# Optimization experiments

Measured on AMD Instinct MI355X. Metric: run time of the kernel, lower is better.

## Reference

```python
import jax, jax.numpy as jnp
import numpy as np

MAX_NUM_BINS = 200
BIN_SIZE = 500
NUM_NEIGHBORS = 5
DIST_MULT = 0.1


def setup_inputs() -> dict:
    key = jax.random.key(0)
    k1, k2 = jax.random.split(key)
    points = jax.random.normal(k1, (2, 5000, 128), dtype=jnp.float32)
    rotations = jax.random.normal(k2, (128, MAX_NUM_BINS // 2), dtype=jnp.float32)
    return {"points": points, "rotations": rotations}


def reference(points, rotations):
    # points: [B, N, D], rotations: [D, max_num_bins//2]
    B, N, D = points.shape
    nbins = N // BIN_SIZE  # module requires N % BIN_SIZE == 0

    # LSH bin assignment: project onto nbins//2 random directions, sign-split into nbins bins
    mul = jnp.einsum('bnd,dh->bnh', points, rotations[:, :nbins // 2])  # [B,N,nbins//2]
    cmul = jnp.concatenate([mul, -mul], axis=-1)                        # [B,N,nbins]
    bin_idx = jnp.argmax(cmul, axis=-1)                                 # [B,N]
    # equal-size bins via argsort of bin id (matches tf argsort+reshape)
    bins_split = jnp.argsort(bin_idx, axis=-1).reshape(B, nbins, BIN_SIZE)  # [B,nbins,S]

    # gather points per bin
    parts = jnp.take_along_axis(points, bins_split.reshape(B, N, 1), axis=1)
    parts = parts.reshape(B, nbins, BIN_SIZE, D)

    # per-bin pairwise distance -> gaussian kernel
    na = jnp.sum(parts * parts, axis=-1)                                # [B,nbins,S]
    gram = jnp.einsum('bcid,bcjd->bcij', parts, parts)                  # [B,nbins,S,S]
    dist = jnp.sqrt(jnp.maximum(na[..., :, None] - 2.0 * gram + na[..., None, :], 1e-6))
    dm = jnp.exp(-DIST_MULT * dist)                                     # [B,nbins,S,S]

    # top-k neighbors within each bin
    vals, idx = jax.lax.top_k(dm, NUM_NEIGHBORS)                        # [B,nbins,S,K]

    # map local bin indices back to global point indices
    bs_flat = bins_split.reshape(B * nbins, BIN_SIZE)
    dst = jnp.take_along_axis(bs_flat, idx.reshape(B * nbins, BIN_SIZE * NUM_NEIGHBORS), axis=1)
    dst = dst.reshape(B, nbins, BIN_SIZE, NUM_NEIGHBORS)
    src = jnp.broadcast_to(bins_split[..., None], dst.shape)
    bidx = jnp.broadcast_to(jnp.arange(B)[:, None, None, None], dst.shape)

    # scatter-add into dense [B,N,N] (sparse.add sums duplicate entries)
    out = jnp.zeros((B, N, N), dtype=points.dtype)
    out = out.at[bidx.reshape(-1), src.reshape(-1), dst.reshape(-1)].add(vals.reshape(-1))
    return out
```

## Files before the change

kernel.cpp:

```cpp
#include <hip/hip_runtime.h>
#include <cfloat>
#include <math.h>

#define NPTS   5000
#define BATCH  2
#define DIM    128
#define NBINS  10
#define BINSZ  500
#define TOPK   5
#define ROTCOLS 100

#define KB_PTS 64
#define KB_STR 129
__global__ void k_bins(const float* __restrict__ pts, const float* __restrict__ rot,
                       int* __restrict__ bin_idx, double* __restrict__ na) {
    __shared__ float P[KB_PTS * KB_STR];
    __shared__ float rotL[DIM * 5];
    int tid = threadIdx.x;
    for (int f = tid; f < DIM * 5; f += 256)
        rotL[f] = rot[(f / 5) * ROTCOLS + (f % 5)];

    int p0  = blockIdx.x * KB_PTS;
    int npb = min(KB_PTS, BATCH * NPTS - p0);

    for (int f = tid; f < npb * DIM; f += 256) {
        int r = f >> 7, d = f & 127;
        P[r * KB_STR + d] = pts[(size_t)(p0 + r) * DIM + d];
    }
    __syncthreads();

    int p = tid >> 2;
    int s = tid & 3;
    double acc[5] = {0., 0., 0., 0., 0.};
    double sq = 0.;
    const float* row = &P[p * KB_STR + s * 32];
    for (int j = 0; j < 32; ++j) {
        double v = (double)row[j];
        sq += v * v;
        int d = s * 32 + j;
#pragma unroll
        for (int h = 0; h < 5; ++h) acc[h] += v * (double)rotL[d * 5 + h];
    }
#pragma unroll
    for (int m = 1; m < 4; m <<= 1) {
#pragma unroll
        for (int h = 0; h < 5; ++h) acc[h] += __shfl_xor(acc[h], m, 4);
        sq += __shfl_xor(sq, m, 4);
    }
    if (s == 0 && p < npb) {
        double best = acc[0]; int bc = 0;
#pragma unroll
        for (int c = 1; c < NBINS; ++c) {
            double v = (c < 5) ? acc[c] : -acc[c - 5];
            if (v > best) { best = v; bc = c; }
        }
        bin_idx[p0 + p] = bc;
        na[p0 + p] = sq;
    }
}

__global__ void k_sort(const int* __restrict__ bin_idx, int* __restrict__ order) {
    const int b = blockIdx.x;
    const int t = threadIdx.x;
    const int NPT = (NPTS + 255) / 256;
    int start = t * NPT;
    int end   = min(NPTS, start + NPT);

    int cnt[NBINS];
#pragma unroll
    for (int c = 0; c < NBINS; ++c) cnt[c] = 0;
    for (int i = start; i < end; ++i) {
        int c = bin_idx[b * NPTS + i];
#pragma unroll
        for (int k = 0; k < NBINS; ++k) cnt[k] += (c == k);
    }

    __shared__ int hist[NBINS * 256];
#pragma unroll
    for (int c = 0; c < NBINS; ++c) hist[c * 256 + t] = cnt[c];
    __syncthreads();

    int base = t * NBINS;
    int s = 0;
#pragma unroll
    for (int k = 0; k < NBINS; ++k) s += hist[base + k];
    __shared__ int scan[256];
    scan[t] = s;
    __syncthreads();
    for (int off = 1; off < 256; off <<= 1) {
        int v = (t >= off) ? scan[t - off] : 0;
        __syncthreads();
        scan[t] += v;
        __syncthreads();
    }
    int run = scan[t] - s;
#pragma unroll
    for (int k = 0; k < NBINS; ++k) { int h = hist[base + k]; hist[base + k] = run; run += h; }
    __syncthreads();

    int ofs[NBINS];
#pragma unroll
    for (int c = 0; c < NBINS; ++c) ofs[c] = hist[c * 256 + t];
    for (int i = start; i < end; ++i) {
        int c = bin_idx[b * NPTS + i];
        int pos = 0;
#pragma unroll
        for (int k = 0; k < NBINS; ++k) {
            if (c == k) pos = ofs[k];
            ofs[k] += (c == k);
        }
        order[b * NPTS + pos] = i;
    }
}

#define RT    16
#define NRT   32
#define CTILE 64
#define RSTRD 130
#define CSTR  132
#define NCT   8
#define ROWQ  (NPTS/4)

__launch_bounds__(256, 3)
__global__ void k_chunks(const float* __restrict__ pts, const double* __restrict__ na,
                         const int* __restrict__ order, float* __restrict__ out) {
    __shared__ double rowPd[RT * RSTRD];
    __shared__ float  colP[CTILE * CSTR];
    __shared__ double naC[CTILE];
    __shared__ double naRs[RT];
    __shared__ int    ordR[RT];

    int blk   = blockIdx.x;
    int rt    = blk & (NRT - 1);
    int chunk = blk >> 5;
    int b     = chunk / NBINS;
    int c     = chunk % NBINS;
    int tid   = threadIdx.x;
    int row0  = rt * RT;
    int rowCount = min(RT, BINSZ - row0);

    const int*   ordBase = order + b * NPTS + c * BINSZ;
    const float* ptsB    = pts + (size_t)b * NPTS * DIM;

    for (int f = tid; f < rowCount * (DIM / 4); f += 256) {
        int r = f >> 5;
        int q = f & 31;
        int g = ordBase[row0 + r];
        float4 v = *(const float4*)(ptsB + (size_t)g * DIM + q * 4);
        double2 d01; d01.x = (double)v.x; d01.y = (double)v.y;
        double2 d23; d23.x = (double)v.z; d23.y = (double)v.w;
        *(double2*)(&rowPd[r * RSTRD + q * 4 + 0]) = d01;
        *(double2*)(&rowPd[r * RSTRD + q * 4 + 2]) = d23;
    }
    if (tid < rowCount) {
        int g = ordBase[row0 + tid];
        ordR[tid] = g;
        naRs[tid] = na[b * NPTS + g];
    }
    __syncthreads();

    int rg = tid >> 5;
    int cg = tid & 31;

    double naRr0 = (rg     < rowCount) ? naRs[rg]     : 0.;
    double naRr1 = (rg + 8 < rowCount) ? naRs[rg + 8] : 0.;

    double tv[2][TOPK];
    int    tl[2][TOPK];
#pragma unroll
    for (int ii = 0; ii < 2; ++ii)
#pragma unroll
        for (int k = 0; k < TOPK; ++k) { tv[ii][k] = DBL_MAX; tl[ii][k] = 0x7fffffff; }

    const int totalZ = rowCount * ROWQ;

    for (int ct = 0; ct < NCT; ++ct) {
        int col0 = ct * CTILE;
        int colCount = min(CTILE, BINSZ - col0);
        __syncthreads();
        for (int f = tid; f < colCount * (DIM / 4); f += 256) {
            int j = f >> 5;
            int q = f & 31;
            int g = ordBase[col0 + j];
            float4 v = *(const float4*)(ptsB + (size_t)g * DIM + q * 4);
            *(float4*)(&colP[j * CSTR + q * 4]) = v;
        }
        if (tid < colCount) {
            int g = ordBase[col0 + tid];
            naC[tid] = na[b * NPTS + g];
        }
        __syncthreads();

        {
            float4 z = make_float4(0.f, 0.f, 0.f, 0.f);
            int z0 = (ct * totalZ) / NCT, z1 = ((ct + 1) * totalZ) / NCT;
            for (int f = z0 + tid; f < z1; f += 256) {
                int r = f / ROWQ;
                int q = f - r * ROWQ;
                float* outRow = out + ((size_t)b * NPTS + ordR[r]) * NPTS;
                *(float4*)(outRow + 4 * q) = z;
            }
        }

        double acc00 = 0., acc01 = 0., acc10 = 0., acc11 = 0.;

        for (int q = 0; q < DIM / 4; ++q) {
            double2 a0lo = *(const double2*)(&rowPd[rg * RSTRD + q * 4 + 0]);
            double2 a0hi = *(const double2*)(&rowPd[rg * RSTRD + q * 4 + 2]);
            double2 a1lo = *(const double2*)(&rowPd[(rg + 8) * RSTRD + q * 4 + 0]);
            double2 a1hi = *(const double2*)(&rowPd[(rg + 8) * RSTRD + q * 4 + 2]);
            float4 b0 = *(const float4*)(&colP[cg * CSTR + q * 4]);
            float4 b1 = *(const float4*)(&colP[(cg + 32) * CSTR + q * 4]);
            double b00 = (double)b0.x, b01 = (double)b0.y,
                   b02 = (double)b0.z, b03 = (double)b0.w;
            double b10 = (double)b1.x, b11 = (double)b1.y,
                   b12 = (double)b1.z, b13 = (double)b1.w;
            acc00 += a0lo.x * b00 + a0lo.y * b01 + a0hi.x * b02 + a0hi.y * b03;
            acc01 += a0lo.x * b10 + a0lo.y * b11 + a0hi.x * b12 + a0hi.y * b13;
            acc10 += a1lo.x * b00 + a1lo.y * b01 + a1hi.x * b02 + a1hi.y * b03;
            acc11 += a1lo.x * b10 + a1lo.y * b11 + a1hi.x * b12 + a1hi.y * b13;
        }

#pragma unroll
        for (int jj = 0; jj < 2; ++jj) {
            int j = cg + 32 * jj;
            if (j < colCount) {
                int    cl = col0 + j;
                double nc = naC[j];
                double a0 = (jj == 0) ? acc00 : acc01;
                double a1 = (jj == 0) ? acc10 : acc11;
                double cv0 = fmax(naRr0 + nc - 2. * a0, 1e-6);
                double cv1 = fmax(naRr1 + nc - 2. * a1, 1e-6);
                int cl0 = cl, cl1 = cl;
#pragma unroll
                for (int k = 0; k < TOPK; ++k) {
                    bool lt0 = (cv0 < tv[0][k]);
                    double ov0 = tv[0][k]; int ol0 = tl[0][k];
                    if (lt0) { tv[0][k] = cv0; tl[0][k] = cl0; cv0 = ov0; cl0 = ol0; }
                    bool lt1 = (cv1 < tv[1][k]);
                    double ov1 = tv[1][k]; int ol1 = tl[1][k];
                    if (lt1) { tv[1][k] = cv1; tl[1][k] = cl1; cv1 = ov1; cl1 = ol1; }
                }
            }
        }
    }

#pragma unroll
    for (int m = 1; m < 32; m <<= 1) {
#pragma unroll
        for (int ii = 0; ii < 2; ++ii) {
            double rv[TOPK]; int rl[TOPK];
#pragma unroll
            for (int k = 0; k < TOPK; ++k) {
                rv[k] = __shfl_xor(tv[ii][k], m, 32);
                rl[k] = __shfl_xor(tl[ii][k], m, 32);
            }
#pragma unroll
            for (int k = 0; k < TOPK; ++k) {
                double cv = rv[k]; int cl = rl[k];
#pragma unroll
                for (int s = 0; s < TOPK; ++s) {
                    bool better = (cv < tv[ii][s]) || (cv == tv[ii][s] && cl < tl[ii][s]);
                    double ov = tv[ii][s]; int ol = tl[ii][s];
                    if (better) { tv[ii][s] = cv; tl[ii][s] = cl; cv = ov; cl = ol; }
                }
            }
        }
    }

    __syncthreads();

    if (cg == 0) {
#pragma unroll
        for (int ii = 0; ii < 2; ++ii) {
            int r = rg + 8 * ii;
            if (r < rowCount) {
                int src = ordR[r];
                float* outRow = out + ((size_t)b * NPTS + src) * NPTS;
#pragma unroll
                for (int k = 0; k < TOPK; ++k) {
                    double dist = sqrt(tv[ii][k]);
                    double dm   = exp(-0.1 * dist);
                    int dst = ordBase[tl[ii][k]];
                    outRow[dst] = (float)dm;
                }
            }
        }
    }
}

extern "C" void kernel_launch(void* const* d_in, const int* in_sizes, int n_in,
                              void* d_out, int out_size, void* d_ws, size_t ws_size,
                              hipStream_t stream) {
    const float* pts = (const float*)d_in[0];
    const float* rot = (const float*)d_in[1];
    float* out = (float*)d_out;

    double* na      = (double*)d_ws;
    int*    bin_idx = (int*)((char*)d_ws + 80000);
    int*    order   = (int*)((char*)d_ws + 120000);

    k_bins<<<(BATCH * NPTS + KB_PTS - 1) / KB_PTS, 256, 0, stream>>>(pts, rot, bin_idx, na);
    k_sort<<<BATCH, 256, 0, stream>>>(bin_idx, order);
    k_chunks<<<BATCH * NBINS * NRT, 256, 0, stream>>>(pts, na, order, out);
}
```

Before: 295.5 us.

## Compute per-bin Gram tiles with FP64 MFMA and merge top-k across waves

Replaces the scalar FP64 dot-product loop in the chunk kernel with v_mfma_f64_16x16x4f64 matrix instructions. Each wave computes a 16x16 tile of rows by columns. A runtime probe detects the MFMA operand layout, and a scalar fallback is kept in case the probe fails. The per-row top-k is now reduced over 16-lane shuffles and then merged across the four waves through shared memory. The aim is to cut FP64 ALU cost in the Gram computation, at the price of extra probe work, an additional barrier and a cross-wave merge step.

New measurement: 340.8 us. +15.3%, slower.

```diff
diff --git a/kernel.cpp b/kernel.cpp
--- a/kernel.cpp
+++ b/kernel.cpp
@@ -121,6 +121,8 @@
 #define NCT   8
 #define ROWQ  (NPTS/4)
 
+typedef double v4d __attribute__((ext_vector_type(4)));
+
 __launch_bounds__(256, 3)
 __global__ void k_chunks(const float* __restrict__ pts, const double* __restrict__ na,
                          const int* __restrict__ order, float* __restrict__ out) {
@@ -141,6 +143,31 @@
 
     const int*   ordBase = order + b * NPTS + c * BINSZ;
     const float* ptsB    = pts + (size_t)b * NPTS * DIM;
+
+    int lane = tid & 63;
+    int w    = tid >> 6;
+    int mm   = lane & 15;
+    int gg   = lane >> 4;
+
+    v4d pz = {0., 0., 0., 0.};
+    v4d pB = __builtin_amdgcn_mfma_f64_16x16x4f64(1.0, (double)lane, pz, 0, 0, 0);
+    v4d pA = __builtin_amdgcn_mfma_f64_16x16x4f64((double)lane, 1.0, pz, 0, 0, 0);
+    bool okB1 = true, okB2 = true, okA1 = true, okA2 = true;
+#pragma unroll
+    for (int r = 0; r < 4; ++r) {
+        okB1 = okB1 && (pB[r] == (double)(4 * mm + 96));
+        okB2 = okB2 && (pB[r] == (double)(16 * mm + 6));
+        int rowr = 4 * gg + r;
+        okA1 = okA1 && (pA[r] == (double)(4 * rowr + 96));
+        okA2 = okA2 && (pA[r] == (double)(16 * rowr + 6));
+    }
+    int aconv = __all(okA1) ? 1 : (__all(okA2) ? 2 : 0);
+    int bconv = __all(okB1) ? 1 : (__all(okB2) ? 2 : 0);
+    bool useMfma = (aconv != 0) && (bconv != 0);
+    int iA = (aconv == 2) ? (lane >> 2) : mm;
+    int kA = (aconv == 2) ? (lane & 3)  : gg;
+    int jB = (bconv == 2) ? (lane >> 2) : mm;
+    int kB = (bconv == 2) ? (lane & 3)  : gg;
 
     for (int f = tid; f < rowCount * (DIM / 4); f += 256) {
         int r = f >> 5;
@@ -159,20 +186,24 @@
     }
     __syncthreads();
 
-    int rg = tid >> 5;
-    int cg = tid & 31;
-
-    double naRr0 = (rg     < rowCount) ? naRs[rg]     : 0.;
-    double naRr1 = (rg + 8 < rowCount) ? naRs[rg + 8] : 0.;
-
-    double tv[2][TOPK];
-    int    tl[2][TOPK];
-#pragma unroll
-    for (int ii = 0; ii < 2; ++ii)
-#pragma unroll
-        for (int k = 0; k < TOPK; ++k) { tv[ii][k] = DBL_MAX; tl[ii][k] = 0x7fffffff; }
+    double naR[4];
+#pragma unroll
+    for (int i = 0; i < 4; ++i) {
+        int r = 4 * gg + i;
+        naR[i] = (r < rowCount) ? naRs[r] : 0.;
+    }
+
+    double tv[4][TOPK];
+    int    tl[4][TOPK];
+#pragma unroll
+    for (int i = 0; i < 4; ++i)
+#pragma unroll
+        for (int k = 0; k < TOPK; ++k) { tv[i][k] = DBL_MAX; tl[i][k] = 0x7fffffff; }
 
     const int totalZ = rowCount * ROWQ;
+
+    const double* aBase = &rowPd[iA * RSTRD + kA];
+    const float*  bBase = &colP[(16 * w + jB) * CSTR + kB];
 
     for (int ct = 0; ct < NCT; ++ct) {
         int col0 = ct * CTILE;
@@ -202,89 +233,120 @@
             }
         }
 
-        double acc00 = 0., acc01 = 0., acc10 = 0., acc11 = 0.;
-
-        for (int q = 0; q < DIM / 4; ++q) {
-            double2 a0lo = *(const double2*)(&rowPd[rg * RSTRD + q * 4 + 0]);
-            double2 a0hi = *(const double2*)(&rowPd[rg * RSTRD + q * 4 + 2]);
-            double2 a1lo = *(const double2*)(&rowPd[(rg + 8) * RSTRD + q * 4 + 0]);
-            double2 a1hi = *(const double2*)(&rowPd[(rg + 8) * RSTRD + q * 4 + 2]);
-            float4 b0 = *(const float4*)(&colP[cg * CSTR + q * 4]);
-            float4 b1 = *(const float4*)(&colP[(cg + 32) * CSTR + q * 4]);
-            double b00 = (double)b0.x, b01 = (double)b0.y,
-                   b02 = (double)b0.z, b03 = (double)b0.w;
-            double b10 = (double)b1.x, b11 = (double)b1.y,
-                   b12 = (double)b1.z, b13 = (double)b1.w;
-            acc00 += a0lo.x * b00 + a0lo.y * b01 + a0hi.x * b02 + a0hi.y * b03;
-            acc01 += a0lo.x * b10 + a0lo.y * b11 + a0hi.x * b12 + a0hi.y * b13;
-            acc10 += a1lo.x * b00 + a1lo.y * b01 + a1hi.x * b02 + a1hi.y * b03;
-            acc11 += a1lo.x * b10 + a1lo.y * b11 + a1hi.x * b12 + a1hi.y * b13;
-        }
-
-#pragma unroll
-        for (int jj = 0; jj < 2; ++jj) {
-            int j = cg + 32 * jj;
+        v4d accv = {0., 0., 0., 0.};
+        if (useMfma) {
+#pragma unroll
+            for (int s = 0; s < 32; ++s) {
+                double av = aBase[4 * s];
+                double bv = (double)bBase[4 * s];
+                accv = __builtin_amdgcn_mfma_f64_16x16x4f64(av, bv, accv, 0, 0, 0);
+            }
+        } else {
+            const float*  bcol = &colP[(16 * w + mm) * CSTR];
+            const double* r0 = &rowPd[(4 * gg + 0) * RSTRD];
+            const double* r1 = &rowPd[(4 * gg + 1) * RSTRD];
+            const double* r2 = &rowPd[(4 * gg + 2) * RSTRD];
+            const double* r3 = &rowPd[(4 * gg + 3) * RSTRD];
+            double s0 = 0., s1 = 0., s2 = 0., s3 = 0.;
+#pragma unroll 4
+            for (int q = 0; q < DIM; q += 4) {
+                float4 bf = *(const float4*)(&bcol[q]);
+                double b0 = (double)bf.x, b1 = (double)bf.y,
+                       b2 = (double)bf.z, b3 = (double)bf.w;
+                s0 += r0[q] * b0 + r0[q + 1] * b1 + r0[q + 2] * b2 + r0[q + 3] * b3;
+                s1 += r1[q] * b0 + r1[q + 1] * b1 + r1[q + 2] * b2 + r1[q + 3] * b3;
+                s2 += r2[q] * b0 + r2[q + 1] * b1 + r2[q + 2] * b2 + r2[q + 3] * b3;
+                s3 += r3[q] * b0 + r3[q + 1] * b1 + r3[q + 2] * b2 + r3[q + 3] * b3;
+            }
+            accv[0] = s0; accv[1] = s1; accv[2] = s2; accv[3] = s3;
+        }
+
+        {
+            int j = 16 * w + mm;
             if (j < colCount) {
                 int    cl = col0 + j;
                 double nc = naC[j];
-                double a0 = (jj == 0) ? acc00 : acc01;
-                double a1 = (jj == 0) ? acc10 : acc11;
-                double cv0 = fmax(naRr0 + nc - 2. * a0, 1e-6);
-                double cv1 = fmax(naRr1 + nc - 2. * a1, 1e-6);
-                int cl0 = cl, cl1 = cl;
-#pragma unroll
-                for (int k = 0; k < TOPK; ++k) {
-                    bool lt0 = (cv0 < tv[0][k]);
-                    double ov0 = tv[0][k]; int ol0 = tl[0][k];
-                    if (lt0) { tv[0][k] = cv0; tl[0][k] = cl0; cv0 = ov0; cl0 = ol0; }
-                    bool lt1 = (cv1 < tv[1][k]);
-                    double ov1 = tv[1][k]; int ol1 = tl[1][k];
-                    if (lt1) { tv[1][k] = cv1; tl[1][k] = cl1; cv1 = ov1; cl1 = ol1; }
+#pragma unroll
+                for (int i = 0; i < 4; ++i) {
+                    double cv = fmax(naR[i] + nc - 2. * accv[i], 1e-6);
+                    int ci = cl;
+#pragma unroll
+                    for (int k = 0; k < TOPK; ++k) {
+                        bool lt = (cv < tv[i][k]);
+                        double ov = tv[i][k]; int ol = tl[i][k];
+                        if (lt) { tv[i][k] = cv; tl[i][k] = ci; cv = ov; ci = ol; }
+                    }
                 }
             }
         }
     }
 
 #pragma unroll
-    for (int m = 1; m < 32; m <<= 1) {
-#pragma unroll
-        for (int ii = 0; ii < 2; ++ii) {
+    for (int m = 1; m < 16; m <<= 1) {
+#pragma unroll
+        for (int i = 0; i < 4; ++i) {
             double rv[TOPK]; int rl[TOPK];
 #pragma unroll
             for (int k = 0; k < TOPK; ++k) {
-                rv[k] = __shfl_xor(tv[ii][k], m, 32);
-                rl[k] = __shfl_xor(tl[ii][k], m, 32);
+                rv[k] = __shfl_xor(tv[i][k], m, 16);
+                rl[k] = __shfl_xor(tl[i][k], m, 16);
             }
 #pragma unroll
             for (int k = 0; k < TOPK; ++k) {
                 double cv = rv[k]; int cl = rl[k];
 #pragma unroll
                 for (int s = 0; s < TOPK; ++s) {
-                    bool better = (cv < tv[ii][s]) || (cv == tv[ii][s] && cl < tl[ii][s]);
-                    double ov = tv[ii][s]; int ol = tl[ii][s];
-                    if (better) { tv[ii][s] = cv; tl[ii][s] = cl; cv = ov; cl = ol; }
+                    bool better = (cv < tv[i][s]) || (cv == tv[i][s] && cl < tl[i][s]);
+                    double ov = tv[i][s]; int ol = tl[i][s];
+                    if (better) { tv[i][s] = cv; tl[i][s] = cl; cv = ov; cl = ol; }
                 }
             }
         }
     }
 
     __syncthreads();
-
-    if (cg == 0) {
-#pragma unroll
-        for (int ii = 0; ii < 2; ++ii) {
-            int r = rg + 8 * ii;
-            if (r < rowCount) {
-                int src = ordR[r];
-                float* outRow = out + ((size_t)b * NPTS + src) * NPTS;
-#pragma unroll
-                for (int k = 0; k < TOPK; ++k) {
-                    double dist = sqrt(tv[ii][k]);
-                    double dm   = exp(-0.1 * dist);
-                    int dst = ordBase[tl[ii][k]];
-                    outRow[dst] = (float)dm;
+    double* mV = rowPd;
+    int*    mI = reinterpret_cast<int*>(rowPd + 320);
+    if (mm == 0) {
+#pragma unroll
+        for (int i = 0; i < 4; ++i) {
+            int r = 4 * gg + i;
+#pragma unroll
+            for (int k = 0; k < TOPK; ++k) {
+                mV[(w * RT + r) * TOPK + k] = tv[i][k];
+                mI[(w * RT + r) * TOPK + k] = tl[i][k];
+            }
+        }
+    }
+    __syncthreads();
+
+    if (tid < RT && tid < rowCount) {
+        int r = tid;
+        double fv[TOPK]; int fl[TOPK];
+#pragma unroll
+        for (int k = 0; k < TOPK; ++k) { fv[k] = DBL_MAX; fl[k] = 0x7fffffff; }
+#pragma unroll
+        for (int ww = 0; ww < 4; ++ww) {
+#pragma unroll
+            for (int k = 0; k < TOPK; ++k) {
+                double cv = mV[(ww * RT + r) * TOPK + k];
+                int    cl = mI[(ww * RT + r) * TOPK + k];
+#pragma unroll
+                for (int s = 0; s < TOPK; ++s) {
+                    bool better = (cv < fv[s]) || (cv == fv[s] && cl < fl[s]);
+                    double ov = fv[s]; int ol = fl[s];
+                    if (better) { fv[s] = cv; fl[s] = cl; cv = ov; cl = ol; }
                 }
             }
+        }
+        int src = ordR[r];
+        float* outRow = out + ((size_t)b * NPTS + src) * NPTS;
+#pragma unroll
+        for (int k = 0; k < TOPK; ++k) {
+            double dist = sqrt(fv[k]);
+            double dm   = exp(-0.1 * dist);
+            int dst = ordBase[fl[k]];
+            outRow[dst] = (float)dm;
         }
     }
 }
```

## Compute per-bin gram tiles with FP64 MFMA after runtime layout probe

Applied to the files above, without the earlier changes.

Replaces the scalar FP64 FMA gram-matrix loop with __builtin_amdgcn_mfma_f64_16x16x4f64. Each wave computes a 16x16 tile, and per-lane top-k results are merged through shared memory. At kernel start, probe MFMA calls with lane-index inputs detect the operand and output lane layout, and the kernel falls back to the old scalar path if the layout is not recognized. The aim is to cut FP64 ALU cost in the distance computation, at the price of extra probe work, a serial 256-entry merge per row, and a larger code body.

Measured after the change: 297.0 us. No clear change (+0.5%).

```diff
diff --git a/kernel.cpp b/kernel.cpp
--- a/kernel.cpp
+++ b/kernel.cpp
@@ -121,6 +121,8 @@
 #define NCT   8
 #define ROWQ  (NPTS/4)
 
+typedef double v4d __attribute__((ext_vector_type(4)));
+
 __launch_bounds__(256, 3)
 __global__ void k_chunks(const float* __restrict__ pts, const double* __restrict__ na,
                          const int* __restrict__ order, float* __restrict__ out) {
@@ -141,6 +143,56 @@
 
     const int*   ordBase = order + b * NPTS + c * BINSZ;
     const float* ptsB    = pts + (size_t)b * NPTS * DIM;
+
+    int lane = tid & 63;
+    int w    = tid >> 6;
+    int mm   = lane & 15;
+    int gg   = lane >> 4;
+
+    v4d z4 = {0., 0., 0., 0.};
+    v4d pB  = __builtin_amdgcn_mfma_f64_16x16x4f64(1.0, (double)lane, z4, 0, 0, 0);
+    v4d pA  = __builtin_amdgcn_mfma_f64_16x16x4f64((double)lane, 1.0, z4, 0, 0, 0);
+    v4d pAB = __builtin_amdgcn_mfma_f64_16x16x4f64((double)lane, (double)lane, z4, 0, 0, 0);
+
+    bool ok = true;
+    int aconv = 0, bconv = 0;
+    int rw[4], cj[4];
+#pragma unroll
+    for (int r = 0; r < 4; ++r) {
+        int av = (int)pA[r];
+        ok = ok && ((double)av == pA[r]);
+        int arow = 0, acv = -1;
+        if (av >= 96 && av <= 156 && (av & 3) == 0)       { arow = (av - 96) >> 2; acv = 1; }
+        else if (av >= 6 && av <= 246 && (av & 15) == 6)  { arow = (av - 6) >> 4;  acv = 2; }
+        else ok = false;
+        if (aconv == 0) aconv = acv; else ok = ok && (acv == aconv);
+        rw[r] = arow;
+
+        int bv = (int)pB[r];
+        ok = ok && ((double)bv == pB[r]);
+        int bcol = 0, bcv = -1;
+        if (bv >= 96 && bv <= 156 && (bv & 3) == 0)       { bcol = (bv - 96) >> 2; bcv = 1; }
+        else if (bv >= 6 && bv <= 246 && (bv & 15) == 6)  { bcol = (bv - 6) >> 4;  bcv = 2; }
+        else ok = false;
+        if (bconv == 0) bconv = bcv; else ok = ok && (bcv == bconv);
+        cj[r] = bcol;
+    }
+#pragma unroll
+    for (int r = 0; r < 4; ++r) {
+        double e = 0.;
+#pragma unroll
+        for (int k = 0; k < 4; ++k) {
+            double Aval = (aconv == 2) ? (double)(4 * rw[r] + k) : (double)(16 * k + rw[r]);
+            double Bval = (bconv == 2) ? (double)(4 * cj[r] + k) : (double)(16 * k + cj[r]);
+            e += Aval * Bval;
+        }
+        ok = ok && (pAB[r] == e);
+    }
+    ok = ok && (rw[0] == rw[1] && rw[1] == rw[2] && rw[2] == rw[3]);
+    ok = ok && (cj[0] != cj[1] && cj[0] != cj[2] && cj[0] != cj[3] &&
+                cj[1] != cj[2] && cj[1] != cj[3] && cj[2] != cj[3]);
+    bool useMfma = __all(ok) != 0;
+    int rowL = rw[0];
 
     for (int f = tid; f < rowCount * (DIM / 4); f += 256) {
         int r = f >> 5;
@@ -159,130 +211,236 @@
     }
     __syncthreads();
 
-    int rg = tid >> 5;
-    int cg = tid & 31;
-
-    double naRr0 = (rg     < rowCount) ? naRs[rg]     : 0.;
-    double naRr1 = (rg + 8 < rowCount) ? naRs[rg + 8] : 0.;
-
-    double tv[2][TOPK];
-    int    tl[2][TOPK];
-#pragma unroll
-    for (int ii = 0; ii < 2; ++ii)
-#pragma unroll
-        for (int k = 0; k < TOPK; ++k) { tv[ii][k] = DBL_MAX; tl[ii][k] = 0x7fffffff; }
-
     const int totalZ = rowCount * ROWQ;
 
-    for (int ct = 0; ct < NCT; ++ct) {
-        int col0 = ct * CTILE;
-        int colCount = min(CTILE, BINSZ - col0);
+    if (useMfma) {
+        int iA = (aconv == 2) ? (lane >> 2) : mm;
+        int kA = (aconv == 2) ? (lane & 3)  : gg;
+        int jB = (bconv == 2) ? (lane >> 2) : mm;
+        int kB = (bconv == 2) ? (lane & 3)  : gg;
+        const double* aBase = &rowPd[iA * RSTRD + kA];
+        const float*  bBase = &colP[(16 * w + jB) * CSTR + kB];
+
+        double naRow = naRs[rowL];
+
+        double tv[TOPK]; int tl[TOPK];
+#pragma unroll
+        for (int k = 0; k < TOPK; ++k) { tv[k] = DBL_MAX; tl[k] = 0x7fffffff; }
+
+        for (int ct = 0; ct < NCT; ++ct) {
+            int col0 = ct * CTILE;
+            int colCount = min(CTILE, BINSZ - col0);
+            __syncthreads();
+            for (int f = tid; f < colCount * (DIM / 4); f += 256) {
+                int j = f >> 5;
+                int q = f & 31;
+                int g = ordBase[col0 + j];
+                float4 v = *(const float4*)(ptsB + (size_t)g * DIM + q * 4);
+                *(float4*)(&colP[j * CSTR + q * 4]) = v;
+            }
+            if (tid < colCount) {
+                int g = ordBase[col0 + tid];
+                naC[tid] = na[b * NPTS + g];
+            }
+            __syncthreads();
+
+            {
+                float4 z = make_float4(0.f, 0.f, 0.f, 0.f);
+                int z0 = (ct * totalZ) / NCT, z1 = ((ct + 1) * totalZ) / NCT;
+                for (int f = z0 + tid; f < z1; f += 256) {
+                    int r = f / ROWQ;
+                    int q = f - r * ROWQ;
+                    float* outRow = out + ((size_t)b * NPTS + ordR[r]) * NPTS;
+                    *(float4*)(outRow + 4 * q) = z;
+                }
+            }
+
+            v4d acc = {0., 0., 0., 0.};
+#pragma unroll
+            for (int s = 0; s < 32; ++s) {
+                double av = aBase[4 * s];
+                double bv = (double)bBase[4 * s];
+                acc = __builtin_amdgcn_mfma_f64_16x16x4f64(av, bv, acc, 0, 0, 0);
+            }
+
+#pragma unroll
+            for (int r = 0; r < 4; ++r) {
+                int j16 = 16 * w + cj[r];
+                if (j16 < colCount) {
+                    int    ci = col0 + j16;
+                    double cv = fmax(naRow + naC[j16] - 2. * acc[r], 1e-6);
+#pragma unroll
+                    for (int k = 0; k < TOPK; ++k) {
+                        bool better = (cv < tv[k]) || (cv == tv[k] && ci < tl[k]);
+                        double ov = tv[k]; int ol = tl[k];
+                        if (better) { tv[k] = cv; tl[k] = ci; cv = ov; ci = ol; }
+                    }
+                }
+            }
+        }
+
         __syncthreads();
-        for (int f = tid; f < colCount * (DIM / 4); f += 256) {
-            int j = f >> 5;
-            int q = f & 31;
-            int g = ordBase[col0 + j];
-            float4 v = *(const float4*)(ptsB + (size_t)g * DIM + q * 4);
-            *(float4*)(&colP[j * CSTR + q * 4]) = v;
-        }
-        if (tid < colCount) {
-            int g = ordBase[col0 + tid];
-            naC[tid] = na[b * NPTS + g];
-        }
+        double* mV = rowPd;
+        int*    mI = reinterpret_cast<int*>(rowPd + 1280);
+        int*    mR = reinterpret_cast<int*>(rowPd + 1920);
+#pragma unroll
+        for (int k = 0; k < TOPK; ++k) { mV[tid * TOPK + k] = tv[k]; mI[tid * TOPK + k] = tl[k]; }
+        mR[tid] = rowL;
         __syncthreads();
 
-        {
-            float4 z = make_float4(0.f, 0.f, 0.f, 0.f);
-            int z0 = (ct * totalZ) / NCT, z1 = ((ct + 1) * totalZ) / NCT;
-            for (int f = z0 + tid; f < z1; f += 256) {
-                int r = f / ROWQ;
-                int q = f - r * ROWQ;
-                float* outRow = out + ((size_t)b * NPTS + ordR[r]) * NPTS;
-                *(float4*)(outRow + 4 * q) = z;
-            }
-        }
-
-        double acc00 = 0., acc01 = 0., acc10 = 0., acc11 = 0.;
-
-        for (int q = 0; q < DIM / 4; ++q) {
-            double2 a0lo = *(const double2*)(&rowPd[rg * RSTRD + q * 4 + 0]);
-            double2 a0hi = *(const double2*)(&rowPd[rg * RSTRD + q * 4 + 2]);
-            double2 a1lo = *(const double2*)(&rowPd[(rg + 8) * RSTRD + q * 4 + 0]);
-            double2 a1hi = *(const double2*)(&rowPd[(rg + 8) * RSTRD + q * 4 + 2]);
-            float4 b0 = *(const float4*)(&colP[cg * CSTR + q * 4]);
-            float4 b1 = *(const float4*)(&colP[(cg + 32) * CSTR + q * 4]);
-            double b00 = (double)b0.x, b01 = (double)b0.y,
-                   b02 = (double)b0.z, b03 = (double)b0.w;
-            double b10 = (double)b1.x, b11 = (double)b1.y,
-                   b12 = (double)b1.z, b13 = (double)b1.w;
-            acc00 += a0lo.x * b00 + a0lo.y * b01 + a0hi.x * b02 + a0hi.y * b03;
-            acc01 += a0lo.x * b10 + a0lo.y * b11 + a0hi.x * b12 + a0hi.y * b13;
-            acc10 += a1lo.x * b00 + a1lo.y * b01 + a1hi.x * b02 + a1hi.y * b03;
-            acc11 += a1lo.x * b10 + a1lo.y * b11 + a1hi.x * b12 + a1hi.y * b13;
-        }
-
-#pragma unroll
-        for (int jj = 0; jj < 2; ++jj) {
-            int j = cg + 32 * jj;
-            if (j < colCount) {
-                int    cl = col0 + j;
-                double nc = naC[j];
-                double a0 = (jj == 0) ? acc00 : acc01;
-                double a1 = (jj == 0) ? acc10 : acc11;
-                double cv0 = fmax(naRr0 + nc - 2. * a0, 1e-6);
-                double cv1 = fmax(naRr1 + nc - 2. * a1, 1e-6);
-                int cl0 = cl, cl1 = cl;
+        if (tid < RT && tid < rowCount) {
+            double fv[TOPK]; int fl[TOPK];
+#pragma unroll
+            for (int k = 0; k < TOPK; ++k) { fv[k] = DBL_MAX; fl[k] = 0x7fffffff; }
+            for (int src = 0; src < 256; ++src) {
+                if (mR[src] == tid) {
+#pragma unroll
+                    for (int k = 0; k < TOPK; ++k) {
+                        double cv = mV[src * TOPK + k];
+                        int    cl = mI[src * TOPK + k];
+#pragma unroll
+                        for (int s = 0; s < TOPK; ++s) {
+                            bool better = (cv < fv[s]) || (cv == fv[s] && cl < fl[s]);
+                            double ov = fv[s]; int ol = fl[s];
+                            if (better) { fv[s] = cv; fl[s] = cl; cv = ov; cl = ol; }
+                        }
+                    }
+                }
+            }
+            int src = ordR[tid];
+            float* outRow = out + ((size_t)b * NPTS + src) * NPTS;
+#pragma unroll
+            for (int k = 0; k < TOPK; ++k) {
+                double dist = sqrt(fv[k]);
+                double dm   = exp(-0.1 * dist);
+                int dst = ordBase[fl[k]];
+                outRow[dst] = (float)dm;
+            }
+        }
+    } else {
+        int rg = tid >> 5;
+        int cg = tid & 31;
+
+        double naRr0 = (rg     < rowCount) ? naRs[rg]     : 0.;
+        double naRr1 = (rg + 8 < rowCount) ? naRs[rg + 8] : 0.;
+
+        double tv[2][TOPK];
+        int    tl[2][TOPK];
+#pragma unroll
+        for (int ii = 0; ii < 2; ++ii)
+#pragma unroll
+            for (int k = 0; k < TOPK; ++k) { tv[ii][k] = DBL_MAX; tl[ii][k] = 0x7fffffff; }
+
+        for (int ct = 0; ct < NCT; ++ct) {
+            int col0 = ct * CTILE;
+            int colCount = min(CTILE, BINSZ - col0);
+            __syncthreads();
+            for (int f = tid; f < colCount * (DIM / 4); f += 256) {
+                int j = f >> 5;
+                int q = f & 31;
+                int g = ordBase[col0 + j];
+                float4 v = *(const float4*)(ptsB + (size_t)g * DIM + q * 4);
+                *(float4*)(&colP[j * CSTR + q * 4]) = v;
+            }
+            if (tid < colCount) {
+                int g = ordBase[col0 + tid];
+                naC[tid] = na[b * NPTS + g];
+            }
+            __syncthreads();
+
+            {
+                float4 z = make_float4(0.f, 0.f, 0.f, 0.f);
+                int z0 = (ct * totalZ) / NCT, z1 = ((ct + 1) * totalZ) / NCT;
+                for (int f = z0 + tid; f < z1; f += 256) {
+                    int r = f / ROWQ;
+                    int q = f - r * ROWQ;
+                    float* outRow = out + ((size_t)b * NPTS + ordR[r]) * NPTS;
+                    *(float4*)(outRow + 4 * q) = z;
+                }
+            }
+
+            double acc00 = 0., acc01 = 0., acc10 = 0., acc11 = 0.;
+
+            for (int q = 0; q < DIM / 4; ++q) {
+                double2 a0lo = *(const double2*)(&rowPd[rg * RSTRD + q * 4 + 0]);
+                double2 a0hi = *(const double2*)(&rowPd[rg * RSTRD + q * 4 + 2]);
+                double2 a1lo = *(const double2*)(&rowPd[(rg + 8) * RSTRD + q * 4 + 0]);
+                double2 a1hi = *(const double2*)(&rowPd[(rg + 8) * RSTRD + q * 4 + 2]);
+                float4 b0 = *(const float4*)(&colP[cg * CSTR + q * 4]);
+                float4 b1 = *(const float4*)(&colP[(cg + 32) * CSTR + q * 4]);
+                double b00 = (double)b0.x, b01 = (double)b0.y,
+                       b02 = (double)b0.z, b03 = (double)b0.w;
+                double b10 = (double)b1.x, b11 = (double)b1.y,
+                       b12 = (double)b1.z, b13 = (double)b1.w;
+                acc00 += a0lo.x * b00 + a0lo.y * b01 + a0hi.x * b02 + a0hi.y * b03;
+                acc01 += a0lo.x * b10 + a0lo.y * b11 + a0hi.x * b12 + a0hi.y * b13;
+                acc10 += a1lo.x * b00 + a1lo.y * b01 + a1hi.x * b02 + a1hi.y * b03;
+                acc11 += a1lo.x * b10 + a1lo.y * b11 + a1hi.x * b12 + a1hi.y * b13;
+            }
+
+#pragma unroll
+            for (int jj = 0; jj < 2; ++jj) {
+                int j = cg + 32 * jj;
+                if (j < colCount) {
+                    int    cl = col0 + j;
+                    double nc = naC[j];
+                    double a0 = (jj == 0) ? acc00 : acc01;
+                    double a1 = (jj == 0) ? acc10 : acc11;
+                    double cv0 = fmax(naRr0 + nc - 2. * a0, 1e-6);
+                    double cv1 = fmax(naRr1 + nc - 2. * a1, 1e-6);
+                    int cl0 = cl, cl1 = cl;
+#pragma unroll
+                    for (int k = 0; k < TOPK; ++k) {
+                        bool lt0 = (cv0 < tv[0][k]);
+                        double ov0 = tv[0][k]; int ol0 = tl[0][k];
+                        if (lt0) { tv[0][k] = cv0; tl[0][k] = cl0; cv0 = ov0; cl0 = ol0; }
+                        bool lt1 = (cv1 < tv[1][k]);
+                        double ov1 = tv[1][k]; int ol1 = tl[1][k];
+                        if (lt1) { tv[1][k] = cv1; tl[1][k] = cl1; cv1 = ov1; cl1 = ol1; }
+                    }
+                }
+            }
+        }
+
+#pragma unroll
+        for (int m = 1; m < 32; m <<= 1) {
+#pragma unroll
+            for (int ii = 0; ii < 2; ++ii) {
+                double rv[TOPK]; int rl[TOPK];
 #pragma unroll
                 for (int k = 0; k < TOPK; ++k) {
-                    bool lt0 = (cv0 < tv[0][k]);
-                    double ov0 = tv[0][k]; int ol0 = tl[0][k];
-                    if (lt0) { tv[0][k] = cv0; tl[0][k] = cl0; cv0 = ov0; cl0 = ol0; }
-                    bool lt1 = (cv1 < tv[1][k]);
-                    double ov1 = tv[1][k]; int ol1 = tl[1][k];
-                    if (lt1) { tv[1][k] = cv1; tl[1][k] = cl1; cv1 = ov1; cl1 = ol1; }
-                }
-            }
-        }
-    }
-
-#pragma unroll
-    for (int m = 1; m < 32; m <<= 1) {
-#pragma unroll
-        for (int ii = 0; ii < 2; ++ii) {
-            double rv[TOPK]; int rl[TOPK];
-#pragma unroll
-            for (int k = 0; k < TOPK; ++k) {
-                rv[k] = __shfl_xor(tv[ii][k], m, 32);
-                rl[k] = __shfl_xor(tl[ii][k], m, 32);
-            }
-#pragma unroll
-            for (int k = 0; k < TOPK; ++k) {
-                double cv = rv[k]; int cl = rl[k];
-#pragma unroll
-                for (int s = 0; s < TOPK; ++s) {
-                    bool better = (cv < tv[ii][s]) || (cv == tv[ii][s] && cl < tl[ii][s]);
-                    double ov = tv[ii][s]; int ol = tl[ii][s];
-                    if (better) { tv[ii][s] = cv; tl[ii][s] = cl; cv = ov; cl = ol; }
-                }
-            }
-        }
-    }
-
-    __syncthreads();
-
-    if (cg == 0) {
-#pragma unroll
-        for (int ii = 0; ii < 2; ++ii) {
-            int r = rg + 8 * ii;
-            if (r < rowCount) {
-                int src = ordR[r];
-                float* outRow = out + ((size_t)b * NPTS + src) * NPTS;
+                    rv[k] = __shfl_xor(tv[ii][k], m, 32);
+                    rl[k] = __shfl_xor(tl[ii][k], m, 32);
+                }
 #pragma unroll
                 for (int k = 0; k < TOPK; ++k) {
-                    double dist = sqrt(tv[ii][k]);
-                    double dm   = exp(-0.1 * dist);
-                    int dst = ordBase[tl[ii][k]];
-                    outRow[dst] = (float)dm;
+                    double cv = rv[k]; int cl = rl[k];
+#pragma unroll
+                    for (int s = 0; s < TOPK; ++s) {
+                        bool better = (cv < tv[ii][s]) || (cv == tv[ii][s] && cl < tl[ii][s]);
+                        double ov = tv[ii][s]; int ol = tl[ii][s];
+                        if (better) { tv[ii][s] = cv; tl[ii][s] = cl; cv = ov; cl = ol; }
+                    }
+                }
+            }
+        }
+
+        __syncthreads();
+
+        if (cg == 0) {
+#pragma unroll
+            for (int ii = 0; ii < 2; ++ii) {
+                int r = rg + 8 * ii;
+                if (r < rowCount) {
+                    int src = ordR[r];
+                    float* outRow = out + ((size_t)b * NPTS + src) * NPTS;
+#pragma unroll
+                    for (int k = 0; k < TOPK; ++k) {
+                        double dist = sqrt(tv[ii][k]);
+                        double dm   = exp(-0.1 * dist);
+                        int dst = ordBase[tl[ii][k]];
+                        outRow[dst] = (float)dm;
+                    }
                 }
             }
         }
```

## Split K dimension across half-warps with shuffle reduction in distance GEMM

Applied to the files above, without the earlier changes.

Changes the per-thread tile of the in-bin gram computation: each 32-lane group now splits the 128-long dot product into two halves of 64, with each thread computing 2 rows by 4 columns over its half. Partial sums are combined with an xor-16 shuffle, and each half-lane then handles two of the four columns for the top-k insertion. The goal is more independent FP64 accumulators and better reuse of the row operands loaded from LDS per iteration, at the cost of extra shuffles and more registers. Top-k lanes keep the same 32-lane grouping, so the later merge is unchanged.

Measured after the change: 294.5 us. No clear change (-0.3%).

```diff
diff --git a/kernel.cpp b/kernel.cpp
--- a/kernel.cpp
+++ b/kernel.cpp
@@ -159,8 +159,11 @@
     }
     __syncthreads();
 
-    int rg = tid >> 5;
-    int cg = tid & 31;
+    int cg  = tid & 15;
+    int ks  = (tid >> 4) & 1;
+    int rg  = tid >> 5;
+    int cgm = tid & 31;
+    const int q0 = ks * 64;
 
     double naRr0 = (rg     < rowCount) ? naRs[rg]     : 0.;
     double naRr1 = (rg + 8 < rowCount) ? naRs[rg + 8] : 0.;
@@ -175,18 +178,18 @@
     const int totalZ = rowCount * ROWQ;
 
     for (int ct = 0; ct < NCT; ++ct) {
-        int col0 = ct * CTILE;
-        int colCount = min(CTILE, BINSZ - col0);
+        int col0T = ct * CTILE;
+        int colCount = min(CTILE, BINSZ - col0T);
         __syncthreads();
         for (int f = tid; f < colCount * (DIM / 4); f += 256) {
             int j = f >> 5;
             int q = f & 31;
-            int g = ordBase[col0 + j];
+            int g = ordBase[col0T + j];
             float4 v = *(const float4*)(ptsB + (size_t)g * DIM + q * 4);
             *(float4*)(&colP[j * CSTR + q * 4]) = v;
         }
         if (tid < colCount) {
-            int g = ordBase[col0 + tid];
+            int g = ordBase[col0T + tid];
             naC[tid] = na[b * NPTS + g];
         }
         __syncthreads();
@@ -202,45 +205,79 @@
             }
         }
 
-        double acc00 = 0., acc01 = 0., acc10 = 0., acc11 = 0.;
-
-        for (int q = 0; q < DIM / 4; ++q) {
-            double2 a0lo = *(const double2*)(&rowPd[rg * RSTRD + q * 4 + 0]);
-            double2 a0hi = *(const double2*)(&rowPd[rg * RSTRD + q * 4 + 2]);
-            double2 a1lo = *(const double2*)(&rowPd[(rg + 8) * RSTRD + q * 4 + 0]);
-            double2 a1hi = *(const double2*)(&rowPd[(rg + 8) * RSTRD + q * 4 + 2]);
-            float4 b0 = *(const float4*)(&colP[cg * CSTR + q * 4]);
-            float4 b1 = *(const float4*)(&colP[(cg + 32) * CSTR + q * 4]);
-            double b00 = (double)b0.x, b01 = (double)b0.y,
-                   b02 = (double)b0.z, b03 = (double)b0.w;
-            double b10 = (double)b1.x, b11 = (double)b1.y,
-                   b12 = (double)b1.z, b13 = (double)b1.w;
-            acc00 += a0lo.x * b00 + a0lo.y * b01 + a0hi.x * b02 + a0hi.y * b03;
-            acc01 += a0lo.x * b10 + a0lo.y * b11 + a0hi.x * b12 + a0hi.y * b13;
-            acc10 += a1lo.x * b00 + a1lo.y * b01 + a1hi.x * b02 + a1hi.y * b03;
-            acc11 += a1lo.x * b10 + a1lo.y * b11 + a1hi.x * b12 + a1hi.y * b13;
-        }
-
-#pragma unroll
-        for (int jj = 0; jj < 2; ++jj) {
-            int j = cg + 32 * jj;
-            if (j < colCount) {
-                int    cl = col0 + j;
-                double nc = naC[j];
-                double a0 = (jj == 0) ? acc00 : acc01;
-                double a1 = (jj == 0) ? acc10 : acc11;
-                double cv0 = fmax(naRr0 + nc - 2. * a0, 1e-6);
-                double cv1 = fmax(naRr1 + nc - 2. * a1, 1e-6);
-                int cl0 = cl, cl1 = cl;
-#pragma unroll
-                for (int k = 0; k < TOPK; ++k) {
-                    bool lt0 = (cv0 < tv[0][k]);
-                    double ov0 = tv[0][k]; int ol0 = tl[0][k];
-                    if (lt0) { tv[0][k] = cv0; tl[0][k] = cl0; cv0 = ov0; cl0 = ol0; }
-                    bool lt1 = (cv1 < tv[1][k]);
-                    double ov1 = tv[1][k]; int ol1 = tl[1][k];
-                    if (lt1) { tv[1][k] = cv1; tl[1][k] = cl1; cv1 = ov1; cl1 = ol1; }
-                }
+        double acc00 = 0., acc01 = 0., acc02 = 0., acc03 = 0.;
+        double acc10 = 0., acc11 = 0., acc12 = 0., acc13 = 0.;
+
+        for (int q = 0; q < 64; q += 4) {
+            const int qq = q0 + q;
+            double2 a0lo = *(const double2*)(&rowPd[rg * RSTRD + qq + 0]);
+            double2 a0hi = *(const double2*)(&rowPd[rg * RSTRD + qq + 2]);
+            double2 a1lo = *(const double2*)(&rowPd[(rg + 8) * RSTRD + qq + 0]);
+            double2 a1hi = *(const double2*)(&rowPd[(rg + 8) * RSTRD + qq + 2]);
+            float4 f0 = *(const float4*)(&colP[cg * CSTR + qq]);
+            float4 f1 = *(const float4*)(&colP[(cg + 16) * CSTR + qq]);
+            float4 f2 = *(const float4*)(&colP[(cg + 32) * CSTR + qq]);
+            float4 f3 = *(const float4*)(&colP[(cg + 48) * CSTR + qq]);
+            double b0x = (double)f0.x, b0y = (double)f0.y, b0z = (double)f0.z, b0w = (double)f0.w;
+            double b1x = (double)f1.x, b1y = (double)f1.y, b1z = (double)f1.z, b1w = (double)f1.w;
+            double b2x = (double)f2.x, b2y = (double)f2.y, b2z = (double)f2.z, b2w = (double)f2.w;
+            double b3x = (double)f3.x, b3y = (double)f3.y, b3z = (double)f3.z, b3w = (double)f3.w;
+            acc00 += a0lo.x * b0x + a0lo.y * b0y + a0hi.x * b0z + a0hi.y * b0w;
+            acc01 += a0lo.x * b1x + a0lo.y * b1y + a0hi.x * b1z + a0hi.y * b1w;
+            acc02 += a0lo.x * b2x + a0lo.y * b2y + a0hi.x * b2z + a0hi.y * b2w;
+            acc03 += a0lo.x * b3x + a0lo.y * b3y + a0hi.x * b3z + a0hi.y * b3w;
+            acc10 += a1lo.x * b0x + a1lo.y * b0y + a1hi.x * b0z + a1hi.y * b0w;
+            acc11 += a1lo.x * b1x + a1lo.y * b1y + a1hi.x * b1z + a1hi.y * b1w;
+            acc12 += a1lo.x * b2x + a1lo.y * b2y + a1hi.x * b2z + a1hi.y * b2w;
+            acc13 += a1lo.x * b3x + a1lo.y * b3y + a1hi.x * b3z + a1hi.y * b3w;
+        }
+
+        acc00 += __shfl_xor(acc00, 16, 64);
+        acc01 += __shfl_xor(acc01, 16, 64);
+        acc02 += __shfl_xor(acc02, 16, 64);
+        acc03 += __shfl_xor(acc03, 16, 64);
+        acc10 += __shfl_xor(acc10, 16, 64);
+        acc11 += __shfl_xor(acc11, 16, 64);
+        acc12 += __shfl_xor(acc12, 16, 64);
+        acc13 += __shfl_xor(acc13, 16, 64);
+
+        double selA0 = ks ? acc02 : acc00;
+        double selA1 = ks ? acc12 : acc10;
+        double selB0 = ks ? acc03 : acc01;
+        double selB1 = ks ? acc13 : acc11;
+        int colA = cg + (ks ? 32 : 0);
+        int colB = cg + (ks ? 48 : 16);
+
+        if (colA < colCount) {
+            int    cl = col0T + colA;
+            double nc = naC[colA];
+            double cv0 = fmax(naRr0 + nc - 2. * selA0, 1e-6);
+            double cv1 = fmax(naRr1 + nc - 2. * selA1, 1e-6);
+            int cl0 = cl, cl1 = cl;
+#pragma unroll
+            for (int k = 0; k < TOPK; ++k) {
+                bool lt0 = (cv0 < tv[0][k]);
+                double ov0 = tv[0][k]; int ol0 = tl[0][k];
+                if (lt0) { tv[0][k] = cv0; tl[0][k] = cl0; cv0 = ov0; cl0 = ol0; }
+                bool lt1 = (cv1 < tv[1][k]);
+                double ov1 = tv[1][k]; int ol1 = tl[1][k];
+                if (lt1) { tv[1][k] = cv1; tl[1][k] = cl1; cv1 = ov1; cl1 = ol1; }
+            }
+        }
+        if (colB < colCount) {
+            int    cl = col0T + colB;
+            double nc = naC[colB];
+            double cv0 = fmax(naRr0 + nc - 2. * selB0, 1e-6);
+            double cv1 = fmax(naRr1 + nc - 2. * selB1, 1e-6);
+            int cl0 = cl, cl1 = cl;
+#pragma unroll
+            for (int k = 0; k < TOPK; ++k) {
+                bool lt0 = (cv0 < tv[0][k]);
+                double ov0 = tv[0][k]; int ol0 = tl[0][k];
+                if (lt0) { tv[0][k] = cv0; tl[0][k] = cl0; cv0 = ov0; cl0 = ol0; }
+                bool lt1 = (cv1 < tv[1][k]);
+                double ov1 = tv[1][k]; int ol1 = tl[1][k];
+                if (lt1) { tv[1][k] = cv1; tl[1][k] = cl1; cv1 = ov1; cl1 = ol1; }
             }
         }
     }
@@ -270,7 +307,7 @@
 
     __syncthreads();
 
-    if (cg == 0) {
+    if (cgm == 0) {
 #pragma unroll
         for (int ii = 0; ii < 2; ++ii) {
             int r = rg + 8 * ii;
```
